# Performance work log

Measured on AMD Instinct MI355X. Metric: run time of the kernel, lower is better.

The kernel has to match this reference:

```python
import jax, jax.numpy as jnp
import numpy as np
from jax import lax

PERM_AD = np.array([3, 0, 1, 6, 4, 2, 7, 8, 5])  # angular-difference kernel permutation
IDX_HD_POS = np.array([0, 3, 6]); IDX_HD_NEG = np.array([2, 5, 8])
IDX_VD_POS = np.array([0, 1, 2]); IDX_VD_NEG = np.array([6, 7, 8])
TOP_K = 1
THETA = 1.0


def conv2d_3x3(x, w, b):
    # x: [B,C,H,W], w: [O,I,3,3], b: [O]; stride 1, padding 1
    out = lax.conv_general_dilated(x, w, window_strides=(1, 1), padding=((1, 1), (1, 1)),
                                   dimension_numbers=('NCHW', 'OIHW', 'NCHW'))
    return out + b[None, :, None, None]


def setup_inputs() -> dict:
    key = jax.random.key(0)
    ks = jax.random.split(key, 12)
    B, C, H, W, E = 16, 64, 128, 128, 5

    def winit(k, shape, fan_in):
        return jax.random.normal(k, shape, jnp.float32) * (1.0 / np.sqrt(fan_in))

    return {
        'x': jax.random.normal(ks[0], (B, C, H, W), jnp.float32),
        'noise': jax.random.normal(ks[1], (B, E), jnp.float32),
        'w_gate': winit(ks[2], (C, E), C), 'b_gate': jnp.zeros((E,), jnp.float32),
        'w_noise': winit(ks[3], (C, E), C), 'b_noise': jnp.zeros((E,), jnp.float32),
        'w1': winit(ks[4], (C, C, 3, 3), C * 9), 'b1': jnp.zeros((C,), jnp.float32),
        'w_cd': winit(ks[5], (C, C, 3, 3), C * 9), 'b_cd': jnp.zeros((C,), jnp.float32),
        'w_hd': winit(ks[6], (C, C, 3), C * 3), 'b_hd': jnp.zeros((C,), jnp.float32),
        'w_vd': winit(ks[7], (C, C, 3), C * 3), 'b_vd': jnp.zeros((C,), jnp.float32),
        'w_ad': winit(ks[8], (C, C, 3, 3), C * 9), 'b_ad': jnp.zeros((C,), jnp.float32),
    }


def reference(x, noise, w_gate, b_gate, w_noise, b_noise,
              w1, b1, w_cd, b_cd, w_hd, b_hd, w_vd, b_vd, w_ad, b_ad):
    B, C, H, W = x.shape
    E = w_gate.shape[1]

    # ---- NoisyTopkRouter on globally pooled features ----
    pooled = x.mean(axis=(2, 3))                      # [B, C]
    logits = pooled @ w_gate + b_gate                 # [B, E]
    noise_logits = pooled @ w_noise + b_noise         # [B, E]
    noisy = logits + noise * jax.nn.softplus(noise_logits)
    topv, topi = lax.top_k(noisy, TOP_K)              # [B, k]
    sparse = jnp.full_like(noisy, -jnp.inf)
    sparse = sparse.at[jnp.arange(B)[:, None], topi].set(topv)
    gates = jax.nn.softmax(sparse, axis=-1)           # [B, E]; 0 for unselected, gate weight otherwise

    # ---- Difference-convolution expert kernels ----
    wcd_f = w_cd.reshape(C, C, 9)
    wcd = wcd_f.at[:, :, 4].add(-wcd_f.sum(-1)).reshape(C, C, 3, 3)   # center = w4 - sum(all)
    whd = jnp.zeros((C, C, 9), x.dtype).at[:, :, IDX_HD_POS].set(w_hd).at[:, :, IDX_HD_NEG].set(-w_hd).reshape(C, C, 3, 3)
    wvd = jnp.zeros((C, C, 9), x.dtype).at[:, :, IDX_VD_POS].set(w_vd).at[:, :, IDX_VD_NEG].set(-w_vd).reshape(C, C, 3, 3)
    wad_f = w_ad.reshape(C, C, 9)
    wad = (wad_f - THETA * wad_f[:, :, PERM_AD]).reshape(C, C, 3, 3)

    outs = jnp.stack([
        conv2d_3x3(x, w1, b1),
        conv2d_3x3(x, wcd, b_cd),
        conv2d_3x3(x, whd, b_hd),
        conv2d_3x3(x, wvd, b_vd),
        conv2d_3x3(x, wad, b_ad),
    ], axis=0)                                        # [E, B, C, H, W]

    # ---- SparseDispatcher.combine: per-example softmax over flattened depth, gate-weighted scatter-add ----
    flat = outs.reshape(E, B, C * H * W)
    sm = jax.nn.softmax(flat, axis=-1)                # softmax over depth dim, as in combine()
    combined = jnp.einsum('ebd,be->bd', sm, gates)    # gates are 0 for non-dispatched (expert,example) pairs
    return combined.reshape(B, C, H, W)
```

## Files before the change

kernel.cpp:

```cpp
#include <hip/hip_runtime.h>
#include <math.h>

#define B_  16
#define C_  64
#define HW_ 128
#define E_  5

typedef __bf16  bf16x8 __attribute__((ext_vector_type(8)));
typedef float   f32x4  __attribute__((ext_vector_type(4)));

#define WS_WEFFB   0
#define WS_BIAS    368640
#define WS_POOL    369920
#define WS_Z       374016
#define WS_EIDX    374080
#define WS_XT      374144
#define WS_EXP     33928576
#define WS_NEED_A  67483008ull
#define WS_NEED_B  33928576ull

static __device__ __forceinline__ unsigned short f2bf(float f) {
    unsigned int u = __float_as_uint(f);
    unsigned int r = (u + 0x7fffu + ((u >> 16) & 1u)) >> 16;
    return (unsigned short)r;
}

__global__ __launch_bounds__(256) void transpose_pool_kernel(
        const float* __restrict__ x, unsigned short* __restrict__ x_t,
        float* __restrict__ pooled) {
    int bid = blockIdx.x;
    int b = bid >> 7, row = bid & 127;
    int t = threadIdx.x;
    int wave = t >> 6, l = t & 63;
    int half = l >> 5;
    int c4 = l & 31;

    __shared__ unsigned short T[128][72];

    const float* xb = x + (size_t)b * (64 * 16384) + row * 128;

    #pragma unroll
    for (int it = 0; it < 8; it++) {
        int ci = wave * 16 + it * 2 + half;
        float4 v = *(const float4*)(xb + (size_t)ci * 16384 + c4 * 4);
        float p = v.x + v.y + v.z + v.w;
        p += __shfl_down(p, 16, 32);
        p += __shfl_down(p, 8, 32);
        p += __shfl_down(p, 4, 32);
        p += __shfl_down(p, 2, 32);
        p += __shfl_down(p, 1, 32);
        if (c4 == 0) atomicAdd(&pooled[b * 64 + ci], p * (1.0f / 16384.0f));
        int colb = c4 * 4;
        T[colb + 0][ci] = f2bf(v.x);
        T[colb + 1][ci] = f2bf(v.y);
        T[colb + 2][ci] = f2bf(v.z);
        T[colb + 3][ci] = f2bf(v.w);
    }
    __syncthreads();

    unsigned short* dst = x_t + ((size_t)(b * 128 + row) * 128) * 64;
    #pragma unroll
    for (int k = 0; k < 4; k++) {
        int chunk = t + k * 256;
        int col = chunk >> 3, c8 = chunk & 7;
        uint4 vv = *(const uint4*)&T[col][c8 * 8];
        *(uint4*)(dst + col * 64 + c8 * 8) = vv;
    }
}

__global__ void route_kernel(const float* __restrict__ pooled,
                             const float* __restrict__ noise,
                             const float* __restrict__ w_gate, const float* __restrict__ b_gate,
                             const float* __restrict__ w_noise, const float* __restrict__ b_noise,
                             int* __restrict__ expert_idx) {
    int b = threadIdx.x;
    if (b >= B_) return;
    float best = -1e30f;
    int bi = 0;
    for (int e = 0; e < E_; e++) {
        float lg = b_gate[e], nz = b_noise[e];
        for (int c = 0; c < C_; c++) {
            float pv = pooled[b * C_ + c];
            lg += pv * w_gate[c * E_ + e];
            nz += pv * w_noise[c * E_ + e];
        }
        float sp = log1pf(expf(nz));
        float v = lg + noise[b * E_ + e] * sp;
        if (v > best) { best = v; bi = e; }
    }
    expert_idx[b] = bi;
}

__global__ void build_w_kernel(const float* __restrict__ w1, const float* __restrict__ w_cd,
                               const float* __restrict__ w_hd, const float* __restrict__ w_vd,
                               const float* __restrict__ w_ad,
                               const float* __restrict__ b1, const float* __restrict__ b_cd,
                               const float* __restrict__ b_hd, const float* __restrict__ b_vd,
                               const float* __restrict__ b_ad,
                               unsigned short* __restrict__ wEffB, float* __restrict__ biasEff) {
    int gid = blockIdx.x * 256 + threadIdx.x;
    if (gid < E_ * 36864) {
        int e   = gid / 36864;
        int r   = gid % 36864;
        int g   = r / 18432;
        int r2  = r % 18432;
        int tap = r2 / 2048;
        int r3  = r2 % 2048;
        int q   = r3 / 512;
        int r4  = r3 % 512;
        int co  = r4 / 8;
        int j   = r4 % 8;
        int ci = g * 32 + q * 8 + j;
        int base9 = (co * 64 + ci) * 9;
        int base3 = (co * 64 + ci) * 3;
        float v = 0.f;
        if (e == 0) {
            v = w1[base9 + tap];
        } else if (e == 1) {
            if (tap == 4) {
                float s = 0.f;
                #pragma unroll
                for (int k = 0; k < 9; k++) s += w_cd[base9 + k];
                v = w_cd[base9 + 4] - s;
            } else {
                v = w_cd[base9 + tap];
            }
        } else if (e == 2) {
            int m = tap % 3;
            if (m == 0) v = w_hd[base3 + tap / 3];
            else if (m == 2) v = -w_hd[base3 + tap / 3];
        } else if (e == 3) {
            if (tap < 3) v = w_vd[base3 + tap];
            else if (tap >= 6) v = -w_vd[base3 + tap - 6];
        } else {
            const int PERM[9] = {3, 0, 1, 6, 4, 2, 7, 8, 5};
            v = w_ad[base9 + tap] - w_ad[base9 + PERM[tap]];
        }
        wEffB[gid] = f2bf(v);
    } else if (gid < E_ * 36864 + E_ * 64) {
        int jj = gid - E_ * 36864;
        int e = jj / 64, co = jj % 64;
        const float* bs;
        switch (e) {
            case 0: bs = b1; break;
            case 1: bs = b_cd; break;
            case 2: bs = b_hd; break;
            case 3: bs = b_vd; break;
            default: bs = b_ad; break;
        }
        biasEff[jj] = bs[co];
    }
}

__global__ __launch_bounds__(256) void conv_mfma_kernel(
        const unsigned short* __restrict__ x_t, const unsigned short* __restrict__ wEffB,
        const float* __restrict__ biasEff, const int* __restrict__ expert_idx,
        unsigned short* __restrict__ expw, float* __restrict__ outf,
        float* __restrict__ Z, int direct_f32) {
    int bid = blockIdx.x;
    int b = bid >> 6;
    int rem = bid & 63;
    int rg = rem >> 1;
    int ch = rem & 1;

    int t = threadIdx.x;
    int wave = t >> 6;
    int lane = t & 63;
    int ln = lane & 15;
    int q = lane >> 4;

    int e = expert_idx[b];

    __shared__ __align__(16) unsigned short A_lds[9 * 4 * 66 * 8];
    __shared__ __align__(16) unsigned short Xs[6 * 4 * 68 * 8];
    __shared__ float zs[4];

    f32x4 acc[4][4];
    #pragma unroll
    for (int i = 0; i < 4; i++)
        #pragma unroll
        for (int jn = 0; jn < 4; jn++)
            acc[i][jn] = (f32x4){0.f, 0.f, 0.f, 0.f};

    const unsigned short* xb = x_t + (size_t)b * (128 * 128 * 64);
    const unsigned short* we = wEffB + (size_t)e * 36864;

    for (int g = 0; g < 2; g++) {
        const uint4* asrc = (const uint4*)(we + g * 18432);
        for (int j = t; j < 2304; j += 256) {
            int slotrow = j >> 6;
            int m = j & 63;
            *(uint4*)&A_lds[(slotrow * 66 + m) * 8] = asrc[j];
        }
        for (int j = t; j < 1584; j += 256) {
            int xr = j / 264;
            int r2 = j % 264;
            int col = r2 >> 2;
            int qq = r2 & 3;
            int irow = rg * 4 - 1 + xr;
            int icol = ch * 64 - 1 + col;
            uint4 v = make_uint4(0, 0, 0, 0);
            if ((unsigned)irow < 128u && (unsigned)icol < 128u)
                v = *(const uint4*)(xb + ((size_t)irow * 128 + icol) * 64 + g * 32 + qq * 8);
            *(uint4*)&Xs[((xr * 4 + qq) * 68 + col) * 8] = v;
        }
        __syncthreads();

        #pragma unroll
        for (int tap = 0; tap < 9; tap++) {
            int dr = tap / 3, dc = tap % 3;
            bf16x8 af[4], bfr[4];
            #pragma unroll
            for (int mt = 0; mt < 4; mt++)
                af[mt] = *(const bf16x8*)&A_lds[((tap * 4 + q) * 66 + mt * 16 + ln) * 8];
            int xr = wave + dr;
            #pragma unroll
            for (int t4 = 0; t4 < 4; t4++)
                bfr[t4] = *(const bf16x8*)&Xs[((xr * 4 + q) * 68 + t4 * 16 + ln + dc) * 8];
            #pragma unroll
            for (int mt = 0; mt < 4; mt++)
                #pragma unroll
                for (int t4 = 0; t4 < 4; t4++)
                    acc[mt][t4] = __builtin_amdgcn_mfma_f32_16x16x32_bf16(
                        af[mt], bfr[t4], acc[mt][t4], 0, 0, 0);
        }
        __syncthreads();
    }

    int orow = rg * 4 + wave;
    float bsum = 0.f;
    size_t obase = (size_t)b * (64 * 16384);
    #pragma unroll
    for (int mt = 0; mt < 4; mt++) {
        float4 bias4 = *(const float4*)(biasEff + e * 64 + mt * 16 + q * 4);
        const float* bp = (const float*)&bias4;
        #pragma unroll
        for (int r = 0; r < 4; r++) {
            int co = mt * 16 + q * 4 + r;
            size_t cb = obase + (size_t)co * 16384 + (size_t)orow * 128;
            #pragma unroll
            for (int t4 = 0; t4 < 4; t4++) {
                float ev = __expf(acc[mt][t4][r] + bp[r]);
                bsum += ev;
                int ocol = ch * 64 + t4 * 16 + ln;
                if (direct_f32) outf[cb + ocol] = ev;
                else            expw[cb + ocol] = f2bf(ev);
            }
        }
    }
    for (int off = 32; off; off >>= 1) bsum += __shfl_down(bsum, off, 64);
    if (lane == 0) zs[wave] = bsum;
    __syncthreads();
    if (t == 0) atomicAdd(&Z[b], zs[0] + zs[1] + zs[2] + zs[3]);
}

__global__ __launch_bounds__(256) void scale_bf16_kernel(
        const unsigned short* __restrict__ expw, const float* __restrict__ Z,
        float* __restrict__ out) {
    int gid = blockIdx.x * 256 + threadIdx.x;
    int b = gid >> 17;
    __shared__ float sinv;
    if (threadIdx.x == 0) sinv = 1.0f / Z[b];
    __syncthreads();
    uint4 r = ((const uint4*)expw)[gid];
    float4 o0, o1;
    o0.x = __uint_as_float(r.x << 16) * sinv;
    o0.y = __uint_as_float(r.x & 0xffff0000u) * sinv;
    o0.z = __uint_as_float(r.y << 16) * sinv;
    o0.w = __uint_as_float(r.y & 0xffff0000u) * sinv;
    o1.x = __uint_as_float(r.z << 16) * sinv;
    o1.y = __uint_as_float(r.z & 0xffff0000u) * sinv;
    o1.z = __uint_as_float(r.w << 16) * sinv;
    o1.w = __uint_as_float(r.w & 0xffff0000u) * sinv;
    ((float4*)out)[gid * 2] = o0;
    ((float4*)out)[gid * 2 + 1] = o1;
}

__global__ __launch_bounds__(256) void scale_inplace_kernel(
        float* __restrict__ out, const float* __restrict__ Z) {
    int gid = blockIdx.x * 256 + threadIdx.x;
    int b = gid >> 18;
    __shared__ float sinv;
    if (threadIdx.x == 0) sinv = 1.0f / Z[b];
    __syncthreads();
    float4 v = ((float4*)out)[gid];
    v.x *= sinv; v.y *= sinv; v.z *= sinv; v.w *= sinv;
    ((float4*)out)[gid] = v;
}

extern "C" void kernel_launch(void* const* d_in, const int* in_sizes, int n_in,
                              void* d_out, int out_size, void* d_ws, size_t ws_size,
                              hipStream_t stream) {
    const float* x       = (const float*)d_in[0];
    const float* noise   = (const float*)d_in[1];
    const float* w_gate  = (const float*)d_in[2];
    const float* b_gate  = (const float*)d_in[3];
    const float* w_noise = (const float*)d_in[4];
    const float* b_noise = (const float*)d_in[5];
    const float* w1      = (const float*)d_in[6];
    const float* b1      = (const float*)d_in[7];
    const float* w_cd    = (const float*)d_in[8];
    const float* b_cd    = (const float*)d_in[9];
    const float* w_hd    = (const float*)d_in[10];
    const float* b_hd    = (const float*)d_in[11];
    const float* w_vd    = (const float*)d_in[12];
    const float* b_vd    = (const float*)d_in[13];
    const float* w_ad    = (const float*)d_in[14];
    const float* b_ad    = (const float*)d_in[15];

    char* ws = (char*)d_ws;
    unsigned short* wEffB   = (unsigned short*)(ws + WS_WEFFB);
    float*          biasEff = (float*)(ws + WS_BIAS);
    float*          pooled  = (float*)(ws + WS_POOL);
    float*          Zbuf    = (float*)(ws + WS_Z);
    int*            eidx    = (int*)(ws + WS_EIDX);
    unsigned short* x_t     = (unsigned short*)(ws + WS_XT);
    unsigned short* expw    = (unsigned short*)(ws + WS_EXP);

    float* out = (float*)d_out;
    int mode_a = (ws_size >= WS_NEED_A) ? 1 : 0;

    hipMemsetAsync(pooled, 0, 4160, stream);

    transpose_pool_kernel<<<B_ * 128, 256, 0, stream>>>(x, x_t, pooled);
    route_kernel<<<1, 64, 0, stream>>>(pooled, noise, w_gate, b_gate, w_noise, b_noise, eidx);
    build_w_kernel<<<(E_ * 36864 + E_ * 64 + 255) / 256, 256, 0, stream>>>(
        w1, w_cd, w_hd, w_vd, w_ad, b1, b_cd, b_hd, b_vd, b_ad, wEffB, biasEff);
    conv_mfma_kernel<<<1024, 256, 0, stream>>>(x_t, wEffB, biasEff, eidx,
                                               expw, out, Zbuf, mode_a ? 0 : 1);
    if (mode_a)
        scale_bf16_kernel<<<8192, 256, 0, stream>>>(expw, Zbuf, out);
    else
        scale_inplace_kernel<<<16384, 256, 0, stream>>>(out, Zbuf);
}
```

Baseline: 229.6 us.

## Drop pooling atomics and memset, swizzle transpose LDS, read conv weights from global

The pooling step now writes per-row partial sums into scratch space at the tail of the output buffer, and the route kernel reduces them with 1024 threads. This removes the atomics and the memset, and the route kernel also zeroes Z. The transpose uses an XOR-swizzled LDS layout instead of padding and writes x_t split by channel half. The conv kernel no longer stages weights in LDS. It reads A fragments straight from global (L2) and sets launch bounds to 4 blocks per CU to raise occupancy, at the cost of more global traffic for the weights.

Measured after the change: 240.1 us. 1.05x slower.

```diff
diff --git a/kernel.cpp b/kernel.cpp
--- a/kernel.cpp
+++ b/kernel.cpp
@@ -17,7 +17,6 @@
 #define WS_XT      374144
 #define WS_EXP     33928576
 #define WS_NEED_A  67483008ull
-#define WS_NEED_B  33928576ull
 
 static __device__ __forceinline__ unsigned short f2bf(float f) {
     unsigned int u = __float_as_uint(f);
@@ -27,7 +26,7 @@
 
 __global__ __launch_bounds__(256) void transpose_pool_kernel(
         const float* __restrict__ x, unsigned short* __restrict__ x_t,
-        float* __restrict__ pooled) {
+        float* __restrict__ partial) {
     int bid = blockIdx.x;
     int b = bid >> 7, row = bid & 127;
     int t = threadIdx.x;
@@ -35,7 +34,7 @@
     int half = l >> 5;
     int c4 = l & 31;
 
-    __shared__ unsigned short T[128][72];
+    __shared__ unsigned short T[128 * 64];
 
     const float* xb = x + (size_t)b * (64 * 16384) + row * 128;
 
@@ -49,46 +48,57 @@
         p += __shfl_down(p, 4, 32);
         p += __shfl_down(p, 2, 32);
         p += __shfl_down(p, 1, 32);
-        if (c4 == 0) atomicAdd(&pooled[b * 64 + ci], p * (1.0f / 16384.0f));
+        if (c4 == 0) partial[((size_t)b * 128 + row) * 64 + ci] = p;
         int colb = c4 * 4;
-        T[colb + 0][ci] = f2bf(v.x);
-        T[colb + 1][ci] = f2bf(v.y);
-        T[colb + 2][ci] = f2bf(v.z);
-        T[colb + 3][ci] = f2bf(v.w);
-    }
-    __syncthreads();
-
-    unsigned short* dst = x_t + ((size_t)(b * 128 + row) * 128) * 64;
+        T[(colb + 0) * 64 + (ci ^ (((colb + 0) & 7) << 3))] = f2bf(v.x);
+        T[(colb + 1) * 64 + (ci ^ (((colb + 1) & 7) << 3))] = f2bf(v.y);
+        T[(colb + 2) * 64 + (ci ^ (((colb + 2) & 7) << 3))] = f2bf(v.z);
+        T[(colb + 3) * 64 + (ci ^ (((colb + 3) & 7) << 3))] = f2bf(v.w);
+    }
+    __syncthreads();
+
+    uint4* dst = (uint4*)x_t;
     #pragma unroll
     for (int k = 0; k < 4; k++) {
         int chunk = t + k * 256;
         int col = chunk >> 3, c8 = chunk & 7;
-        uint4 vv = *(const uint4*)&T[col][c8 * 8];
-        *(uint4*)(dst + col * 64 + c8 * 8) = vv;
-    }
-}
-
-__global__ void route_kernel(const float* __restrict__ pooled,
-                             const float* __restrict__ noise,
-                             const float* __restrict__ w_gate, const float* __restrict__ b_gate,
-                             const float* __restrict__ w_noise, const float* __restrict__ b_noise,
-                             int* __restrict__ expert_idx) {
-    int b = threadIdx.x;
-    if (b >= B_) return;
-    float best = -1e30f;
-    int bi = 0;
-    for (int e = 0; e < E_; e++) {
-        float lg = b_gate[e], nz = b_noise[e];
-        for (int c = 0; c < C_; c++) {
-            float pv = pooled[b * C_ + c];
-            lg += pv * w_gate[c * E_ + e];
-            nz += pv * w_noise[c * E_ + e];
-        }
-        float sp = log1pf(expf(nz));
-        float v = lg + noise[b * E_ + e] * sp;
-        if (v > best) { best = v; bi = e; }
-    }
-    expert_idx[b] = bi;
+        uint4 vv = *(const uint4*)&T[col * 64 + ((c8 * 8) ^ ((col & 7) << 3))];
+        int g = c8 >> 2, qq = c8 & 3;
+        dst[((size_t)(b * 2 + g) * 16384 + row * 128 + col) * 4 + qq] = vv;
+    }
+}
+
+__global__ __launch_bounds__(1024) void route_kernel(
+        const float* __restrict__ partial, const float* __restrict__ noise,
+        const float* __restrict__ w_gate, const float* __restrict__ b_gate,
+        const float* __restrict__ w_noise, const float* __restrict__ b_noise,
+        int* __restrict__ expert_idx, float* __restrict__ Z) {
+    __shared__ float pl[1024];
+    int t = threadIdx.x;
+    int b = t >> 6, ci = t & 63;
+    float s = 0.f;
+    const float* pp = partial + ((size_t)b * 128) * 64 + ci;
+    #pragma unroll 4
+    for (int r = 0; r < 128; r++) s += pp[r * 64];
+    pl[t] = s * (1.0f / 16384.0f);
+    __syncthreads();
+    if (t < B_) {
+        float best = -1e30f;
+        int bi = 0;
+        for (int e = 0; e < E_; e++) {
+            float lg = b_gate[e], nz = b_noise[e];
+            for (int c = 0; c < C_; c++) {
+                float pv = pl[t * 64 + c];
+                lg += pv * w_gate[c * E_ + e];
+                nz += pv * w_noise[c * E_ + e];
+            }
+            float sp = log1pf(expf(nz));
+            float v = lg + noise[t * E_ + e] * sp;
+            if (v > best) { best = v; bi = e; }
+        }
+        expert_idx[t] = bi;
+        Z[t] = 0.f;
+    }
 }
 
 __global__ void build_w_kernel(const float* __restrict__ w1, const float* __restrict__ w_cd,
@@ -152,7 +162,7 @@
     }
 }
 
-__global__ __launch_bounds__(256) void conv_mfma_kernel(
+__global__ __launch_bounds__(256, 4) void conv_mfma_kernel(
         const unsigned short* __restrict__ x_t, const unsigned short* __restrict__ wEffB,
         const float* __restrict__ biasEff, const int* __restrict__ expert_idx,
         unsigned short* __restrict__ expw, float* __restrict__ outf,
@@ -171,7 +181,6 @@
 
     int e = expert_idx[b];
 
-    __shared__ __align__(16) unsigned short A_lds[9 * 4 * 66 * 8];
     __shared__ __align__(16) unsigned short Xs[6 * 4 * 68 * 8];
     __shared__ float zs[4];
 
@@ -182,37 +191,32 @@
         for (int jn = 0; jn < 4; jn++)
             acc[i][jn] = (f32x4){0.f, 0.f, 0.f, 0.f};
 
-    const unsigned short* xb = x_t + (size_t)b * (128 * 128 * 64);
-    const unsigned short* we = wEffB + (size_t)e * 36864;
+    const uint4* xq = (const uint4*)x_t;
 
     for (int g = 0; g < 2; g++) {
-        const uint4* asrc = (const uint4*)(we + g * 18432);
-        for (int j = t; j < 2304; j += 256) {
-            int slotrow = j >> 6;
-            int m = j & 63;
-            *(uint4*)&A_lds[(slotrow * 66 + m) * 8] = asrc[j];
-        }
+        size_t base_g = (size_t)(b * 2 + g) * 16384 * 4;
         for (int j = t; j < 1584; j += 256) {
-            int xr = j / 264;
-            int r2 = j % 264;
-            int col = r2 >> 2;
-            int qq = r2 & 3;
+            int cq = j >> 2;
+            int xr = cq / 66;
+            int col = cq % 66;
+            int qq = j & 3;
             int irow = rg * 4 - 1 + xr;
             int icol = ch * 64 - 1 + col;
             uint4 v = make_uint4(0, 0, 0, 0);
             if ((unsigned)irow < 128u && (unsigned)icol < 128u)
-                v = *(const uint4*)(xb + ((size_t)irow * 128 + icol) * 64 + g * 32 + qq * 8);
+                v = xq[base_g + ((size_t)irow * 128 + icol) * 4 + qq];
             *(uint4*)&Xs[((xr * 4 + qq) * 68 + col) * 8] = v;
         }
         __syncthreads();
 
+        const bf16x8* Ag = (const bf16x8*)(wEffB + (size_t)e * 36864 + g * 18432);
         #pragma unroll
         for (int tap = 0; tap < 9; tap++) {
             int dr = tap / 3, dc = tap % 3;
             bf16x8 af[4], bfr[4];
             #pragma unroll
             for (int mt = 0; mt < 4; mt++)
-                af[mt] = *(const bf16x8*)&A_lds[((tap * 4 + q) * 66 + mt * 16 + ln) * 8];
+                af[mt] = Ag[(tap * 4 + q) * 64 + mt * 16 + ln];
             int xr = wave + dr;
             #pragma unroll
             for (int t4 = 0; t4 < 4; t4++)
@@ -311,19 +315,19 @@
     char* ws = (char*)d_ws;
     unsigned short* wEffB   = (unsigned short*)(ws + WS_WEFFB);
     float*          biasEff = (float*)(ws + WS_BIAS);
-    float*          pooled  = (float*)(ws + WS_POOL);
     float*          Zbuf    = (float*)(ws + WS_Z);
     int*            eidx    = (int*)(ws + WS_EIDX);
     unsigned short* x_t     = (unsigned short*)(ws + WS_XT);
     unsigned short* expw    = (unsigned short*)(ws + WS_EXP);
 
     float* out = (float*)d_out;
+    float* partial = out + (16 * 1024 * 1024 - 128 * 1024);
+
     int mode_a = (ws_size >= WS_NEED_A) ? 1 : 0;
 
-    hipMemsetAsync(pooled, 0, 4160, stream);
-
-    transpose_pool_kernel<<<B_ * 128, 256, 0, stream>>>(x, x_t, pooled);
-    route_kernel<<<1, 64, 0, stream>>>(pooled, noise, w_gate, b_gate, w_noise, b_noise, eidx);
+    transpose_pool_kernel<<<B_ * 128, 256, 0, stream>>>(x, x_t, partial);
+    route_kernel<<<1, 1024, 0, stream>>>(partial, noise, w_gate, b_gate,
+                                         w_noise, b_noise, eidx, Zbuf);
     build_w_kernel<<<(E_ * 36864 + E_ * 64 + 255) / 256, 256, 0, stream>>>(
         w1, w_cd, w_hd, w_vd, w_ad, b1, b_cd, b_hd, b_vd, b_ad, wEffB, biasEff);
     conv_mfma_kernel<<<1024, 256, 0, stream>>>(x_t, wEffB, biasEff, eidx,
```

## Recompute convolution twice instead of storing exp intermediate, use padded channel-plane layout

Applied to the files above, without the earlier changes.

The conv kernel now runs twice: the first pass only accumulates the per-example softmax denominator, and the second recomputes the conv and writes normalized exp directly to the output. This removes the bf16/f32 intermediate buffer and the separate scale kernel. The input transpose now writes a padded 8-channel-plane bf16 layout with zero borders, and tiles load it with global_load_lds. Each block now covers 8 rows with 2 blocks per CU, and the blocks are interleaved across batch. The cost is doubled MFMA work and a second full read of the transposed input.

Measured after the change: 342.0 us. +49.0%, slower.

```diff
diff --git a/kernel.cpp b/kernel.cpp
--- a/kernel.cpp
+++ b/kernel.cpp
@@ -5,6 +5,7 @@
 #define C_  64
 #define HW_ 128
 #define E_  5
+#define PLANE 16640
 
 typedef __bf16  bf16x8 __attribute__((ext_vector_type(8)));
 typedef float   f32x4  __attribute__((ext_vector_type(4)));
@@ -15,9 +16,13 @@
 #define WS_Z       374016
 #define WS_EIDX    374080
 #define WS_XT      374144
-#define WS_EXP     33928576
-#define WS_NEED_A  67483008ull
-#define WS_NEED_B  33928576ull
+
+typedef const __attribute__((address_space(1))) uint4* gas_u4;
+typedef __attribute__((address_space(3))) uint4*       las_u4;
+
+static __device__ __forceinline__ void glds16(const void* g, void* l) {
+    __builtin_amdgcn_global_load_lds((gas_u4)g, (las_u4)l, 16, 0, 0);
+}
 
 static __device__ __forceinline__ unsigned short f2bf(float f) {
     unsigned int u = __float_as_uint(f);
@@ -25,70 +30,78 @@
     return (unsigned short)r;
 }
 
+__global__ __launch_bounds__(256) void border_kernel(uint4* __restrict__ x_t) {
+    int gid = blockIdx.x * 256 + threadIdx.x;
+    int plane = gid >> 8;
+    int rem = gid & 255;
+    int row = rem >> 1, side = rem & 1;
+    x_t[(size_t)plane * PLANE + row * 130 + side * 129] = make_uint4(0, 0, 0, 0);
+}
+
 __global__ __launch_bounds__(256) void transpose_pool_kernel(
-        const float* __restrict__ x, unsigned short* __restrict__ x_t,
+        const float* __restrict__ x, uint4* __restrict__ x_t,
         float* __restrict__ pooled) {
     int bid = blockIdx.x;
     int b = bid >> 7, row = bid & 127;
     int t = threadIdx.x;
-    int wave = t >> 6, l = t & 63;
-    int half = l >> 5;
-    int c4 = l & 31;
-
-    __shared__ unsigned short T[128][72];
-
     const float* xb = x + (size_t)b * (64 * 16384) + row * 128;
 
-    #pragma unroll
-    for (int it = 0; it < 8; it++) {
-        int ci = wave * 16 + it * 2 + half;
-        float4 v = *(const float4*)(xb + (size_t)ci * 16384 + c4 * 4);
-        float p = v.x + v.y + v.z + v.w;
-        p += __shfl_down(p, 16, 32);
-        p += __shfl_down(p, 8, 32);
-        p += __shfl_down(p, 4, 32);
-        p += __shfl_down(p, 2, 32);
-        p += __shfl_down(p, 1, 32);
-        if (c4 == 0) atomicAdd(&pooled[b * 64 + ci], p * (1.0f / 16384.0f));
-        int colb = c4 * 4;
-        T[colb + 0][ci] = f2bf(v.x);
-        T[colb + 1][ci] = f2bf(v.y);
-        T[colb + 2][ci] = f2bf(v.z);
-        T[colb + 3][ci] = f2bf(v.w);
-    }
-    __syncthreads();
-
-    unsigned short* dst = x_t + ((size_t)(b * 128 + row) * 128) * 64;
     #pragma unroll
     for (int k = 0; k < 4; k++) {
-        int chunk = t + k * 256;
-        int col = chunk >> 3, c8 = chunk & 7;
-        uint4 vv = *(const uint4*)&T[col][c8 * 8];
-        *(uint4*)(dst + col * 64 + c8 * 8) = vv;
-    }
-}
-
-__global__ void route_kernel(const float* __restrict__ pooled,
-                             const float* __restrict__ noise,
-                             const float* __restrict__ w_gate, const float* __restrict__ b_gate,
-                             const float* __restrict__ w_noise, const float* __restrict__ b_noise,
-                             int* __restrict__ expert_idx) {
-    int b = threadIdx.x;
-    if (b >= B_) return;
-    float best = -1e30f;
-    int bi = 0;
-    for (int e = 0; e < E_; e++) {
+        int idx = k * 256 + t;
+        int qq8 = idx >> 7;
+        int col = idx & 127;
+        float v[8];
+        #pragma unroll
+        for (int j = 0; j < 8; j++)
+            v[j] = xb[(size_t)(qq8 * 8 + j) * 16384 + col];
+        #pragma unroll
+        for (int j = 0; j < 8; j++) {
+            float s = v[j];
+            s += __shfl_down(s, 32);
+            s += __shfl_down(s, 16);
+            s += __shfl_down(s, 8);
+            s += __shfl_down(s, 4);
+            s += __shfl_down(s, 2);
+            s += __shfl_down(s, 1);
+            if ((t & 63) == 0)
+                atomicAdd(&pooled[b * 64 + qq8 * 8 + j], s * (1.0f / 16384.0f));
+        }
+        uint4 o;
+        o.x = (unsigned)f2bf(v[0]) | ((unsigned)f2bf(v[1]) << 16);
+        o.y = (unsigned)f2bf(v[2]) | ((unsigned)f2bf(v[3]) << 16);
+        o.z = (unsigned)f2bf(v[4]) | ((unsigned)f2bf(v[5]) << 16);
+        o.w = (unsigned)f2bf(v[6]) | ((unsigned)f2bf(v[7]) << 16);
+        x_t[((size_t)b * 8 + qq8) * PLANE + row * 130 + col + 1] = o;
+    }
+}
+
+__global__ __launch_bounds__(256) void route_kernel(
+        const float* __restrict__ pooled, const float* __restrict__ noise,
+        const float* __restrict__ w_gate, const float* __restrict__ b_gate,
+        const float* __restrict__ w_noise, const float* __restrict__ b_noise,
+        int* __restrict__ expert_idx) {
+    __shared__ float vv[16][5];
+    int t = threadIdx.x;
+    if (t < 80) {
+        int b = t / 5, e = t % 5;
         float lg = b_gate[e], nz = b_noise[e];
-        for (int c = 0; c < C_; c++) {
-            float pv = pooled[b * C_ + c];
-            lg += pv * w_gate[c * E_ + e];
-            nz += pv * w_noise[c * E_ + e];
+        for (int c = 0; c < 64; c++) {
+            float pv = pooled[b * 64 + c];
+            lg += pv * w_gate[c * 5 + e];
+            nz += pv * w_noise[c * 5 + e];
         }
         float sp = log1pf(expf(nz));
-        float v = lg + noise[b * E_ + e] * sp;
-        if (v > best) { best = v; bi = e; }
-    }
-    expert_idx[b] = bi;
+        vv[b][e] = lg + noise[b * 5 + e] * sp;
+    }
+    __syncthreads();
+    if (t < 16) {
+        float best = vv[t][0];
+        int bi = 0;
+        for (int e = 1; e < 5; e++)
+            if (vv[t][e] > best) { best = vv[t][e]; bi = e; }
+        expert_idx[t] = bi;
+    }
 }
 
 __global__ void build_w_kernel(const float* __restrict__ w1, const float* __restrict__ w_cd,
@@ -152,140 +165,119 @@
     }
 }
 
-__global__ __launch_bounds__(256) void conv_mfma_kernel(
-        const unsigned short* __restrict__ x_t, const unsigned short* __restrict__ wEffB,
+__global__ __launch_bounds__(256, 2) void conv_mfma_kernel(
+        const uint4* __restrict__ x_t, const unsigned short* __restrict__ wEffB,
         const float* __restrict__ biasEff, const int* __restrict__ expert_idx,
-        unsigned short* __restrict__ expw, float* __restrict__ outf,
-        float* __restrict__ Z, int direct_f32) {
+        float* __restrict__ out, float* __restrict__ Z, int write_out) {
     int bid = blockIdx.x;
-    int b = bid >> 6;
-    int rem = bid & 63;
+    int k8 = bid & 7;
+    int i = bid >> 3;
+    int b = k8 + ((i >> 5) << 3);
+    int rem = i & 31;
     int rg = rem >> 1;
     int ch = rem & 1;
 
     int t = threadIdx.x;
-    int wave = t >> 6;
-    int lane = t & 63;
-    int ln = lane & 15;
-    int q = lane >> 4;
-
+    int wave = t >> 6, lane = t & 63;
+    int ln = lane & 15, q = lane >> 4;
     int e = expert_idx[b];
 
-    __shared__ __align__(16) unsigned short A_lds[9 * 4 * 66 * 8];
-    __shared__ __align__(16) unsigned short Xs[6 * 4 * 68 * 8];
+    __shared__ __align__(16) unsigned short A_lds[2304 * 8];
+    __shared__ __align__(16) unsigned short Xs[2640 * 8];
     __shared__ float zs[4];
 
-    f32x4 acc[4][4];
+    f32x4 acc[4][2][4];
     #pragma unroll
-    for (int i = 0; i < 4; i++)
-        #pragma unroll
-        for (int jn = 0; jn < 4; jn++)
-            acc[i][jn] = (f32x4){0.f, 0.f, 0.f, 0.f};
-
-    const unsigned short* xb = x_t + (size_t)b * (128 * 128 * 64);
+    for (int m = 0; m < 4; m++)
+        #pragma unroll
+        for (int r = 0; r < 2; r++)
+            #pragma unroll
+            for (int n = 0; n < 4; n++)
+                acc[m][r][n] = (f32x4){0.f, 0.f, 0.f, 0.f};
+
     const unsigned short* we = wEffB + (size_t)e * 36864;
+    const uint4 zero4 = make_uint4(0, 0, 0, 0);
 
     for (int g = 0; g < 2; g++) {
-        const uint4* asrc = (const uint4*)(we + g * 18432);
-        for (int j = t; j < 2304; j += 256) {
-            int slotrow = j >> 6;
-            int m = j & 63;
-            *(uint4*)&A_lds[(slotrow * 66 + m) * 8] = asrc[j];
-        }
-        for (int j = t; j < 1584; j += 256) {
-            int xr = j / 264;
-            int r2 = j % 264;
-            int col = r2 >> 2;
-            int qq = r2 & 3;
-            int irow = rg * 4 - 1 + xr;
-            int icol = ch * 64 - 1 + col;
-            uint4 v = make_uint4(0, 0, 0, 0);
-            if ((unsigned)irow < 128u && (unsigned)icol < 128u)
-                v = *(const uint4*)(xb + ((size_t)irow * 128 + icol) * 64 + g * 32 + qq * 8);
-            *(uint4*)&Xs[((xr * 4 + qq) * 68 + col) * 8] = v;
+        for (int r = wave; r < 76; r += 4) {
+            if (r < 36) {
+                const unsigned short* gp = we + (size_t)g * 18432 + (size_t)(r * 64 + lane) * 8;
+                glds16(gp, &A_lds[(r * 64 + lane) * 8]);
+            } else {
+                int ii = r - 36;
+                int xr = ii >> 2;
+                int qq = ii & 3;
+                int prow = rg * 8 - 1 + xr;
+                int sbase = (xr * 4 + qq) * 66;
+                if ((unsigned)prow < 128u) {
+                    size_t gbase = ((size_t)b * 8 + g * 4 + qq) * PLANE + (size_t)prow * 130 + ch * 64;
+                    glds16(&x_t[gbase + lane], &Xs[(sbase + lane) * 8]);
+                    if (lane < 2) {
+                        uint4 v = x_t[gbase + 64 + lane];
+                        *(uint4*)&Xs[(sbase + 64 + lane) * 8] = v;
+                    }
+                } else {
+                    *(uint4*)&Xs[(sbase + lane) * 8] = zero4;
+                    if (lane < 2) *(uint4*)&Xs[(sbase + 64 + lane) * 8] = zero4;
+                }
+            }
         }
         __syncthreads();
 
         #pragma unroll
         for (int tap = 0; tap < 9; tap++) {
             int dr = tap / 3, dc = tap % 3;
-            bf16x8 af[4], bfr[4];
+            bf16x8 af[4];
             #pragma unroll
             for (int mt = 0; mt < 4; mt++)
-                af[mt] = *(const bf16x8*)&A_lds[((tap * 4 + q) * 66 + mt * 16 + ln) * 8];
-            int xr = wave + dr;
+                af[mt] = *(const bf16x8*)&A_lds[((tap * 4 + q) * 64 + mt * 16 + ln) * 8];
             #pragma unroll
-            for (int t4 = 0; t4 < 4; t4++)
-                bfr[t4] = *(const bf16x8*)&Xs[((xr * 4 + q) * 68 + t4 * 16 + ln + dc) * 8];
-            #pragma unroll
-            for (int mt = 0; mt < 4; mt++)
+            for (int r2 = 0; r2 < 2; r2++) {
+                int srow = ((wave * 2 + r2 + dr) * 4 + q) * 66;
                 #pragma unroll
-                for (int t4 = 0; t4 < 4; t4++)
-                    acc[mt][t4] = __builtin_amdgcn_mfma_f32_16x16x32_bf16(
-                        af[mt], bfr[t4], acc[mt][t4], 0, 0, 0);
+                for (int t4 = 0; t4 < 4; t4++) {
+                    bf16x8 bfr = *(const bf16x8*)&Xs[(srow + t4 * 16 + ln + dc) * 8];
+                    #pragma unroll
+                    for (int mt = 0; mt < 4; mt++)
+                        acc[mt][r2][t4] = __builtin_amdgcn_mfma_f32_16x16x32_bf16(
+                            af[mt], bfr, acc[mt][r2][t4], 0, 0, 0);
+                }
+            }
         }
         __syncthreads();
     }
 
-    int orow = rg * 4 + wave;
+    float zinv = write_out ? (1.0f / Z[b]) : 0.f;
     float bsum = 0.f;
-    size_t obase = (size_t)b * (64 * 16384);
     #pragma unroll
     for (int mt = 0; mt < 4; mt++) {
-        float4 bias4 = *(const float4*)(biasEff + e * 64 + mt * 16 + q * 4);
-        const float* bp = (const float*)&bias4;
-        #pragma unroll
-        for (int r = 0; r < 4; r++) {
-            int co = mt * 16 + q * 4 + r;
-            size_t cb = obase + (size_t)co * 16384 + (size_t)orow * 128;
+        float4 b4 = *(const float4*)(biasEff + e * 64 + mt * 16 + q * 4);
+        const float* bp = (const float*)&b4;
+        #pragma unroll
+        for (int r2 = 0; r2 < 2; r2++) {
+            int orow = rg * 8 + wave * 2 + r2;
             #pragma unroll
             for (int t4 = 0; t4 < 4; t4++) {
-                float ev = __expf(acc[mt][t4][r] + bp[r]);
-                bsum += ev;
                 int ocol = ch * 64 + t4 * 16 + ln;
-                if (direct_f32) outf[cb + ocol] = ev;
-                else            expw[cb + ocol] = f2bf(ev);
+                #pragma unroll
+                for (int k = 0; k < 4; k++) {
+                    float ev = __expf(acc[mt][r2][t4][k] + bp[k]);
+                    if (write_out) {
+                        int co = mt * 16 + q * 4 + k;
+                        out[(((size_t)b * 64 + co) * 128 + orow) * 128 + ocol] = ev * zinv;
+                    } else {
+                        bsum += ev;
+                    }
+                }
             }
         }
     }
-    for (int off = 32; off; off >>= 1) bsum += __shfl_down(bsum, off, 64);
-    if (lane == 0) zs[wave] = bsum;
-    __syncthreads();
-    if (t == 0) atomicAdd(&Z[b], zs[0] + zs[1] + zs[2] + zs[3]);
-}
-
-__global__ __launch_bounds__(256) void scale_bf16_kernel(
-        const unsigned short* __restrict__ expw, const float* __restrict__ Z,
-        float* __restrict__ out) {
-    int gid = blockIdx.x * 256 + threadIdx.x;
-    int b = gid >> 17;
-    __shared__ float sinv;
-    if (threadIdx.x == 0) sinv = 1.0f / Z[b];
-    __syncthreads();
-    uint4 r = ((const uint4*)expw)[gid];
-    float4 o0, o1;
-    o0.x = __uint_as_float(r.x << 16) * sinv;
-    o0.y = __uint_as_float(r.x & 0xffff0000u) * sinv;
-    o0.z = __uint_as_float(r.y << 16) * sinv;
-    o0.w = __uint_as_float(r.y & 0xffff0000u) * sinv;
-    o1.x = __uint_as_float(r.z << 16) * sinv;
-    o1.y = __uint_as_float(r.z & 0xffff0000u) * sinv;
-    o1.z = __uint_as_float(r.w << 16) * sinv;
-    o1.w = __uint_as_float(r.w & 0xffff0000u) * sinv;
-    ((float4*)out)[gid * 2] = o0;
-    ((float4*)out)[gid * 2 + 1] = o1;
-}
-
-__global__ __launch_bounds__(256) void scale_inplace_kernel(
-        float* __restrict__ out, const float* __restrict__ Z) {
-    int gid = blockIdx.x * 256 + threadIdx.x;
-    int b = gid >> 18;
-    __shared__ float sinv;
-    if (threadIdx.x == 0) sinv = 1.0f / Z[b];
-    __syncthreads();
-    float4 v = ((float4*)out)[gid];
-    v.x *= sinv; v.y *= sinv; v.z *= sinv; v.w *= sinv;
-    ((float4*)out)[gid] = v;
+    if (!write_out) {
+        for (int off = 32; off; off >>= 1) bsum += __shfl_down(bsum, off);
+        if (lane == 0) zs[wave] = bsum;
+        __syncthreads();
+        if (t == 0) atomicAdd(&Z[b], zs[0] + zs[1] + zs[2] + zs[3]);
+    }
 }
 
 extern "C" void kernel_launch(void* const* d_in, const int* in_sizes, int n_in,
@@ -314,22 +306,18 @@
     float*          pooled  = (float*)(ws + WS_POOL);
     float*          Zbuf    = (float*)(ws + WS_Z);
     int*            eidx    = (int*)(ws + WS_EIDX);
-    unsigned short* x_t     = (unsigned short*)(ws + WS_XT);
-    unsigned short* expw    = (unsigned short*)(ws + WS_EXP);
+    uint4*          x_t     = (uint4*)(ws + WS_XT);
 
     float* out = (float*)d_out;
-    int mode_a = (ws_size >= WS_NEED_A) ? 1 : 0;
 
     hipMemsetAsync(pooled, 0, 4160, stream);
 
+    border_kernel<<<128, 256, 0, stream>>>(x_t);
     transpose_pool_kernel<<<B_ * 128, 256, 0, stream>>>(x, x_t, pooled);
-    route_kernel<<<1, 64, 0, stream>>>(pooled, noise, w_gate, b_gate, w_noise, b_noise, eidx);
-    build_w_kernel<<<(E_ * 36864 + E_ * 64 + 255) / 256, 256, 0, stream>>>(
+    route_kernel<<<1, 256, 0, stream>>>(pooled, noise, w_gate, b_gate,
+                                        w_noise, b_noise, eidx);
+    build_w_kernel<<<722, 256, 0, stream>>>(
         w1, w_cd, w_hd, w_vd, w_ad, b1, b_cd, b_hd, b_vd, b_ad, wEffB, biasEff);
-    conv_mfma_kernel<<<1024, 256, 0, stream>>>(x_t, wEffB, biasEff, eidx,
-                                               expw, out, Zbuf, mode_a ? 0 : 1);
-    if (mode_a)
-        scale_bf16_kernel<<<8192, 256, 0, stream>>>(expw, Zbuf, out);
-    else
-        scale_inplace_kernel<<<16384, 256, 0, stream>>>(out, Zbuf);
-}
+    conv_mfma_kernel<<<512, 256, 0, stream>>>(x_t, wEffB, biasEff, eidx, out, Zbuf, 0);
+    conv_mfma_kernel<<<512, 256, 0, stream>>>(x_t, wEffB, biasEff, eidx, out, Zbuf, 1);
+}
```
